# Kernel optimization log

Measured on AMD Instinct MI355X. Metric: run time of the kernel, lower is better.

## Reference

```python
import jax, jax.numpy as jnp
import numpy as np

N_NODES = 100000
N_EDGES = 1600000
D_FEAT = 128
D_EMB = 128
ROUNDS = 4
M_OUT = 32
NUM_GRAPHS = 512


def setup_inputs() -> dict:
    key = jax.random.key(0)
    ks = jax.random.split(key, 12)
    x = jax.random.normal(ks[0], (N_NODES, D_FEAT), dtype=jnp.float32)
    edge_index = jax.random.randint(ks[1], (2, N_EDGES), 0, N_NODES, dtype=jnp.int32)
    batch = jnp.sort(jax.random.randint(ks[2], (N_NODES,), 0, NUM_GRAPHS, dtype=jnp.int32))
    s = 1.0 / np.sqrt(D_EMB)
    emb_W = jax.random.uniform(ks[3], (D_FEAT, D_EMB), minval=-s, maxval=s, dtype=jnp.float32)
    emb_b = jax.random.uniform(ks[4], (D_EMB,), minval=-s, maxval=s, dtype=jnp.float32)
    msg_W = jax.random.uniform(ks[5], (ROUNDS, D_EMB, D_EMB), minval=-s, maxval=s, dtype=jnp.float32)
    msg_b = jax.random.uniform(ks[6], (ROUNDS, D_EMB), minval=-s, maxval=s, dtype=jnp.float32)
    upd_W = jax.random.uniform(ks[7], (ROUNDS, D_EMB, D_EMB), minval=-s, maxval=s, dtype=jnp.float32)
    upd_b = jax.random.uniform(ks[8], (ROUNDS, D_EMB), minval=-s, maxval=s, dtype=jnp.float32)
    out_W = jax.random.uniform(ks[9], (D_EMB, M_OUT), minval=-s, maxval=s, dtype=jnp.float32)
    out_b = jax.random.uniform(ks[10], (M_OUT,), minval=-s, maxval=s, dtype=jnp.float32)
    return {"x": x, "edge_index": edge_index, "batch": batch,
            "emb_W": emb_W, "emb_b": emb_b, "msg_W": msg_W, "msg_b": msg_b,
            "upd_W": upd_W, "upd_b": upd_b, "out_W": out_W, "out_b": out_b}


def reference(x, edge_index, batch, emb_W, emb_b, msg_W, msg_b, upd_W, upd_b, out_W, out_b):
    src, dst = edge_index[0], edge_index[1]
    # initial node embedding: Linear + ReLU
    state = jax.nn.relu(x @ emb_W + emb_b)  # [N, D]
    for r in range(ROUNDS):
        message = jax.nn.relu(state @ msg_W[r] + msg_b[r])      # [N, D]
        # gather messages along edges, scatter-add to destination nodes
        aggregated = jax.ops.segment_sum(message[src], dst, num_segments=N_NODES)  # [N, D]
        state = state + jax.nn.relu(aggregated @ upd_W[r] + upd_b[r])
    # sum-pool nodes into graphs
    graph_state = jax.ops.segment_sum(state, batch, num_segments=NUM_GRAPHS)  # [G, D]
    return graph_state @ out_W + out_b  # [G, M]
```

## Files before the change

kernel.cpp:

```cpp
#include <hip/hip_runtime.h>

#define N_NODES    100000
#define N_EDGES    1600000
#define D_EMB      128
#define ROUNDS     4
#define M_OUT      32
#define NUM_GRAPHS 512

#define N_TILES    (N_NODES / 32)
#define GEMM_BLOCKS 1024

#define NPASS      8
#define PASS_RANGE (N_NODES / NPASS)

#define SCAN_ELEMS_PER_BLOCK 1024
#define SCAN_NBLK ((N_NODES + SCAN_ELEMS_PER_BLOCK - 1) / SCAN_ELEMS_PER_BLOCK)

typedef __attribute__((ext_vector_type(8))) short short8;
typedef __attribute__((ext_vector_type(4))) float f32x4;

static __device__ __forceinline__ unsigned short f2bf(float f) {
    union { float f; unsigned u; } v; v.f = f;
    unsigned u = v.u;
    unsigned r = (u + 0x7FFFu + ((u >> 16) & 1u)) >> 16;
    return (unsigned short)r;
}
static __device__ __forceinline__ float bf2f(unsigned short h) {
    union { unsigned u; float f; } v; v.u = ((unsigned)h) << 16;
    return v.f;
}

__global__ __launch_bounds__(256) void prep_weights_kernel(
    const float* __restrict__ emb_W, const float* __restrict__ msg_W,
    const float* __restrict__ upd_W, unsigned short* __restrict__ WTall)
{
    const int mi = blockIdx.x;
    const float* W = (mi == 0) ? emb_W
                   : (mi <= 4) ? msg_W + (size_t)(mi - 1) * D_EMB * D_EMB
                               : upd_W + (size_t)(mi - 5) * D_EMB * D_EMB;
    unsigned short* WT = WTall + (size_t)mi * D_EMB * D_EMB;
    for (int idx = threadIdx.x; idx < D_EMB * D_EMB; idx += 256) {
        const int n = idx >> 7, k = idx & 127;
        WT[idx] = f2bf(W[k * D_EMB + n]);
    }
}

template<int MODE, bool AF32>
__global__ __launch_bounds__(256) void gemm_loop_kernel(
    const void* __restrict__ Aptr, const unsigned short* __restrict__ WT,
    const float* __restrict__ bias, unsigned short* __restrict__ state,
    unsigned short* __restrict__ outb)
{
    __shared__ unsigned short As[2][32][136];

    const int tid  = threadIdx.x;
    const int lane = tid & 63;
    const int w    = tid >> 6;
    const int m    = lane & 15;
    const int g    = lane >> 4;

    short8 bfr[2][4];
    #pragma unroll
    for (int ct = 0; ct < 2; ++ct) {
        const int n = w * 32 + ct * 16 + m;
        #pragma unroll
        for (int ks = 0; ks < 4; ++ks)
            bfr[ct][ks] = *(const short8*)&WT[n * D_EMB + ks * 32 + g * 8];
    }
    const float bv0 = bias[w * 32 + m];
    const float bv1 = bias[w * 32 + 16 + m];

    int tile = blockIdx.x;

    if (AF32) {
        const float4* A4 = (const float4*)Aptr;
        #pragma unroll
        for (int i = 0; i < 4; ++i) {
            const int ch = tid + (i << 8);
            const float4 f = A4[(size_t)tile * 1024 + ch];
            ushort4 h; h.x = f2bf(f.x); h.y = f2bf(f.y); h.z = f2bf(f.z); h.w = f2bf(f.w);
            *(ushort4*)&As[0][ch >> 5][(ch & 31) << 2] = h;
        }
    } else {
        const uint4* A2 = (const uint4*)Aptr;
        #pragma unroll
        for (int i = 0; i < 2; ++i) {
            const int ch = tid + (i << 8);
            const uint4 v = A2[(size_t)tile * 512 + ch];
            *(uint4*)&As[0][ch >> 4][(ch & 15) << 3] = v;
        }
    }
    __syncthreads();

    int cur = 0;
    while (true) {
        const int next = tile + GEMM_BLOCKS;
        const bool have = next < N_TILES;

        float4 rgf[4]; uint4 rgu[2];
        if (have) {
            if (AF32) {
                const float4* A4 = (const float4*)Aptr;
                #pragma unroll
                for (int i = 0; i < 4; ++i)
                    rgf[i] = A4[(size_t)next * 1024 + tid + (i << 8)];
            } else {
                const uint4* A2 = (const uint4*)Aptr;
                #pragma unroll
                for (int i = 0; i < 2; ++i)
                    rgu[i] = A2[(size_t)next * 512 + tid + (i << 8)];
            }
        }

        short8 a[2][4];
        #pragma unroll
        for (int rt = 0; rt < 2; ++rt)
            #pragma unroll
            for (int ks = 0; ks < 4; ++ks)
                a[rt][ks] = *(const short8*)&As[cur][rt * 16 + m][ks * 32 + g * 8];

        f32x4 acc[2][2] = {};
        #pragma unroll
        for (int ks = 0; ks < 4; ++ks)
            #pragma unroll
            for (int rt = 0; rt < 2; ++rt)
                #pragma unroll
                for (int ct = 0; ct < 2; ++ct)
                    acc[rt][ct] = __builtin_amdgcn_mfma_f32_16x16x32_bf16(
                        a[rt][ks], bfr[ct][ks], acc[rt][ct], 0, 0, 0);

        if (have) {
            if (AF32) {
                #pragma unroll
                for (int i = 0; i < 4; ++i) {
                    const int ch = tid + (i << 8);
                    ushort4 h;
                    h.x = f2bf(rgf[i].x); h.y = f2bf(rgf[i].y);
                    h.z = f2bf(rgf[i].z); h.w = f2bf(rgf[i].w);
                    *(ushort4*)&As[cur ^ 1][ch >> 5][(ch & 31) << 2] = h;
                }
            } else {
                #pragma unroll
                for (int i = 0; i < 2; ++i) {
                    const int ch = tid + (i << 8);
                    *(uint4*)&As[cur ^ 1][ch >> 4][(ch & 15) << 3] = rgu[i];
                }
            }
        }

        #pragma unroll
        for (int rt = 0; rt < 2; ++rt) {
            #pragma unroll
            for (int ct = 0; ct < 2; ++ct) {
                const int col = w * 32 + ct * 16 + m;
                const float bv = ct ? bv1 : bv0;
                #pragma unroll
                for (int r = 0; r < 4; ++r) {
                    const int row = tile * 32 + rt * 16 + g * 4 + r;
                    const size_t idx = (size_t)row * D_EMB + col;
                    const float v = fmaxf(acc[rt][ct][r] + bv, 0.f);
                    if (MODE == 0) outb[idx] = f2bf(v);
                    else           state[idx] = f2bf(v);
                }
            }
        }

        if (!have) break;
        __syncthreads();
        cur ^= 1;
        tile = next;
    }
}

__global__ __launch_bounds__(256) void hist_mp_kernel(
    const int* __restrict__ dst, int* __restrict__ deg)
{
    const int p = blockIdx.x & 7;
    const int e = (blockIdx.x >> 3) * 256 + threadIdx.x;
    const int d = dst[e];
    if ((unsigned)(d - p * PASS_RANGE) < (unsigned)PASS_RANGE)
        atomicAdd(&deg[d], 1);
}

__global__ __launch_bounds__(256) void scan_local_kernel(
    const int* __restrict__ deg, int* __restrict__ rp, int* __restrict__ partials)
{
    __shared__ int sm[256];
    const int tid  = threadIdx.x;
    const int base = blockIdx.x * SCAN_ELEMS_PER_BLOCK + tid * 4;

    int v0 = (base + 0 < N_NODES) ? deg[base + 0] : 0;
    int v1 = (base + 1 < N_NODES) ? deg[base + 1] : 0;
    int v2 = (base + 2 < N_NODES) ? deg[base + 2] : 0;
    int v3 = (base + 3 < N_NODES) ? deg[base + 3] : 0;
    const int tot = v0 + v1 + v2 + v3;

    sm[tid] = tot;
    __syncthreads();
    #pragma unroll
    for (int off = 1; off < 256; off <<= 1) {
        const int x = (tid >= off) ? sm[tid - off] : 0;
        __syncthreads();
        sm[tid] += x;
        __syncthreads();
    }
    const int bex = sm[tid] - tot;

    if (base + 0 < N_NODES) rp[base + 0] = bex;
    if (base + 1 < N_NODES) rp[base + 1] = bex + v0;
    if (base + 2 < N_NODES) rp[base + 2] = bex + v0 + v1;
    if (base + 3 < N_NODES) rp[base + 3] = bex + v0 + v1 + v2;
    if (tid == 255) partials[blockIdx.x] = sm[255];
}

__global__ __launch_bounds__(128) void scan_partials_kernel(int* __restrict__ partials)
{
    __shared__ int sm[128];
    const int tid = threadIdx.x;
    const int v = (tid < SCAN_NBLK) ? partials[tid] : 0;
    sm[tid] = v;
    __syncthreads();
    #pragma unroll
    for (int off = 1; off < 128; off <<= 1) {
        const int x = (tid >= off) ? sm[tid - off] : 0;
        __syncthreads();
        sm[tid] += x;
        __syncthreads();
    }
    if (tid < SCAN_NBLK) partials[tid] = sm[tid] - v;
}

__global__ __launch_bounds__(256) void scan_fixup_kernel(
    int* __restrict__ rp, const int* __restrict__ partials, int* __restrict__ pos)
{
    const int i = blockIdx.x * 256 + threadIdx.x;
    if (i < N_NODES) {
        const int v = rp[i] + partials[i >> 10];
        rp[i] = v;
        pos[i] = v;
    }
    if (i == 0) rp[N_NODES] = N_EDGES;
}

__global__ __launch_bounds__(256) void fill_mp_kernel(
    const int* __restrict__ src, const int* __restrict__ dst,
    int* __restrict__ pos, int* __restrict__ esrc)
{
    const int p = blockIdx.x & 7;
    const int e = (blockIdx.x >> 3) * 256 + threadIdx.x;
    const int d = dst[e];
    if ((unsigned)(d - p * PASS_RANGE) < (unsigned)PASS_RANGE) {
        const int idx = atomicAdd(&pos[d], 1);
        esrc[idx] = src[e];
    }
}

__global__ __launch_bounds__(256) void fused_upd_kernel(
    const unsigned short* __restrict__ msg, const int* __restrict__ rp,
    const int* __restrict__ esrc, const unsigned short* __restrict__ WT,
    const float* __restrict__ bias, unsigned short* __restrict__ state)
{
    __shared__ unsigned short As[32][136];
    __shared__ int wq;

    const int tid  = threadIdx.x;
    const int lane = tid & 63;
    const int wid  = tid >> 6;
    const int m    = lane & 15;
    const int g    = lane >> 4;
    const int b    = blockIdx.x;
    const int j    = tid & 15;

    if (tid == 0) wq = 0;

    short8 bfr[2][4];
    #pragma unroll
    for (int ct = 0; ct < 2; ++ct) {
        const int n = wid * 32 + ct * 16 + m;
        #pragma unroll
        for (int ks = 0; ks < 4; ++ks)
            bfr[ct][ks] = *(const short8*)&WT[n * D_EMB + ks * 32 + g * 8];
    }
    const float bv0 = bias[wid * 32 + m];
    const float bv1 = bias[wid * 32 + 16 + m];

    __syncthreads();

    const uint4* m4 = (const uint4*)msg;

    while (true) {
        int t = 0;
        if (j == 0) t = atomicAdd(&wq, 1);
        t = __shfl(t, lane & 48, 64);
        if (t >= 32) break;

        const int n = b * 32 + t;
        const int beg = rp[n];
        const int end = rp[n + 1];

        float a0[8] = {0,0,0,0,0,0,0,0};
        float a1[8] = {0,0,0,0,0,0,0,0};
        int i = beg;
        for (; i + 3 < end; i += 4) {
            const uint4 v0 = m4[(size_t)esrc[i]     * 16 + j];
            const uint4 v1 = m4[(size_t)esrc[i + 1] * 16 + j];
            const uint4 v2 = m4[(size_t)esrc[i + 2] * 16 + j];
            const uint4 v3 = m4[(size_t)esrc[i + 3] * 16 + j];
            a0[0] += bf2f(v0.x & 0xffff); a0[1] += bf2f(v0.x >> 16);
            a0[2] += bf2f(v0.y & 0xffff); a0[3] += bf2f(v0.y >> 16);
            a0[4] += bf2f(v0.z & 0xffff); a0[5] += bf2f(v0.z >> 16);
            a0[6] += bf2f(v0.w & 0xffff); a0[7] += bf2f(v0.w >> 16);
            a1[0] += bf2f(v1.x & 0xffff); a1[1] += bf2f(v1.x >> 16);
            a1[2] += bf2f(v1.y & 0xffff); a1[3] += bf2f(v1.y >> 16);
            a1[4] += bf2f(v1.z & 0xffff); a1[5] += bf2f(v1.z >> 16);
            a1[6] += bf2f(v1.w & 0xffff); a1[7] += bf2f(v1.w >> 16);
            a0[0] += bf2f(v2.x & 0xffff); a0[1] += bf2f(v2.x >> 16);
            a0[2] += bf2f(v2.y & 0xffff); a0[3] += bf2f(v2.y >> 16);
            a0[4] += bf2f(v2.z & 0xffff); a0[5] += bf2f(v2.z >> 16);
            a0[6] += bf2f(v2.w & 0xffff); a0[7] += bf2f(v2.w >> 16);
            a1[0] += bf2f(v3.x & 0xffff); a1[1] += bf2f(v3.x >> 16);
            a1[2] += bf2f(v3.y & 0xffff); a1[3] += bf2f(v3.y >> 16);
            a1[4] += bf2f(v3.z & 0xffff); a1[5] += bf2f(v3.z >> 16);
            a1[6] += bf2f(v3.w & 0xffff); a1[7] += bf2f(v3.w >> 16);
        }
        for (; i < end; ++i) {
            const uint4 v0 = m4[(size_t)esrc[i] * 16 + j];
            a0[0] += bf2f(v0.x & 0xffff); a0[1] += bf2f(v0.x >> 16);
            a0[2] += bf2f(v0.y & 0xffff); a0[3] += bf2f(v0.y >> 16);
            a0[4] += bf2f(v0.z & 0xffff); a0[5] += bf2f(v0.z >> 16);
            a0[6] += bf2f(v0.w & 0xffff); a0[7] += bf2f(v0.w >> 16);
        }
        #pragma unroll
        for (int q = 0; q < 8; ++q) a0[q] += a1[q];

        uint4 o;
        o.x = (unsigned)f2bf(a0[0]) | ((unsigned)f2bf(a0[1]) << 16);
        o.y = (unsigned)f2bf(a0[2]) | ((unsigned)f2bf(a0[3]) << 16);
        o.z = (unsigned)f2bf(a0[4]) | ((unsigned)f2bf(a0[5]) << 16);
        o.w = (unsigned)f2bf(a0[6]) | ((unsigned)f2bf(a0[7]) << 16);
        *(uint4*)&As[t][j * 8] = o;
    }
    __syncthreads();

    short8 a[2][4];
    #pragma unroll
    for (int rt = 0; rt < 2; ++rt)
        #pragma unroll
        for (int ks = 0; ks < 4; ++ks)
            a[rt][ks] = *(const short8*)&As[rt * 16 + m][ks * 32 + g * 8];

    f32x4 acc[2][2] = {};
    #pragma unroll
    for (int ks = 0; ks < 4; ++ks)
        #pragma unroll
        for (int rt = 0; rt < 2; ++rt)
            #pragma unroll
            for (int ct = 0; ct < 2; ++ct)
                acc[rt][ct] = __builtin_amdgcn_mfma_f32_16x16x32_bf16(
                    a[rt][ks], bfr[ct][ks], acc[rt][ct], 0, 0, 0);

    #pragma unroll
    for (int rt = 0; rt < 2; ++rt) {
        #pragma unroll
        for (int ct = 0; ct < 2; ++ct) {
            const int col = wid * 32 + ct * 16 + m;
            const float bv = ct ? bv1 : bv0;
            #pragma unroll
            for (int r = 0; r < 4; ++r) {
                const int row = b * 32 + rt * 16 + g * 4 + r;
                const size_t idx = (size_t)row * D_EMB + col;
                const float v = fmaxf(acc[rt][ct][r] + bv, 0.f);
                state[idx] = f2bf(bf2f(state[idx]) + v);
            }
        }
    }
}

__global__ __launch_bounds__(256) void pool_kernel(
    const unsigned short* __restrict__ state, const int* __restrict__ batch,
    float* __restrict__ gs)
{
    const int lane = threadIdx.x & 63;
    const int grp  = threadIdx.x >> 6;
    const int n0 = blockIdx.x * 128 + grp * 32;
    const int c0 = lane * 2;

    float a0 = 0.f, a1 = 0.f;
    int cur = -1;
    for (int i = 0; i < 32; ++i) {
        const int n = n0 + i;
        if (n >= N_NODES) break;
        const int bb = batch[n];
        if (bb != cur) {
            if (cur >= 0) {
                unsafeAtomicAdd(&gs[cur * D_EMB + c0],     a0);
                unsafeAtomicAdd(&gs[cur * D_EMB + c0 + 1], a1);
            }
            cur = bb; a0 = 0.f; a1 = 0.f;
        }
        const unsigned u = *(const unsigned*)&state[(size_t)n * D_EMB + c0];
        a0 += bf2f(u & 0xffff);
        a1 += bf2f(u >> 16);
    }
    if (cur >= 0) {
        unsafeAtomicAdd(&gs[cur * D_EMB + c0],     a0);
        unsafeAtomicAdd(&gs[cur * D_EMB + c0 + 1], a1);
    }
}

__global__ __launch_bounds__(256) void out_kernel(
    const float* __restrict__ gs, const float* __restrict__ W,
    const float* __restrict__ bias, float* __restrict__ out)
{
    const int idx = blockIdx.x * 256 + threadIdx.x;
    const int g = idx >> 5;
    const int m = idx & 31;
    float acc = 0.f;
    #pragma unroll 8
    for (int k = 0; k < D_EMB; ++k)
        acc += gs[g * D_EMB + k] * W[k * M_OUT + m];
    out[idx] = acc + bias[m];
}

extern "C" void kernel_launch(void* const* d_in, const int* in_sizes, int n_in,
                              void* d_out, int out_size, void* d_ws, size_t ws_size,
                              hipStream_t stream)
{
    const float* x     = (const float*)d_in[0];
    const int*   eidx  = (const int*)d_in[1];
    const int*   batch = (const int*)d_in[2];
    const float* emb_W = (const float*)d_in[3];
    const float* emb_b = (const float*)d_in[4];
    const float* msg_W = (const float*)d_in[5];
    const float* msg_b = (const float*)d_in[6];
    const float* upd_W = (const float*)d_in[7];
    const float* upd_b = (const float*)d_in[8];
    const float* out_W = (const float*)d_in[9];
    const float* out_b = (const float*)d_in[10];
    float* out = (float*)d_out;

    const int* src = eidx;
    const int* dst = eidx + N_EDGES;

    char* p = (char*)d_ws;
    unsigned short* state = (unsigned short*)p;   p += (size_t)N_NODES * D_EMB * 2;
    unsigned short* msg   = (unsigned short*)p;   p += (size_t)N_NODES * D_EMB * 2;
    float* gs = (float*)p;                        p += (size_t)NUM_GRAPHS * D_EMB * 4;
    unsigned short* WTall = (unsigned short*)p;   p += (size_t)9 * D_EMB * D_EMB * 2;
    int* rp   = (int*)p;                          p += (size_t)(N_NODES + 1) * 4;
    int* deg  = (int*)p;                          p += (size_t)N_NODES * 4;
    int* pos  = (int*)p;                          p += (size_t)N_NODES * 4;
    int* partials = (int*)p;                      p += (size_t)128 * 4;
    int* esrc = (int*)p;                          p += (size_t)N_EDGES * 4;

    const dim3 blk(256);
    const int mp_grid = (N_EDGES / 256) * NPASS;

    prep_weights_kernel<<<9, blk, 0, stream>>>(emb_W, msg_W, upd_W, WTall);
    hipMemsetAsync(deg, 0, (size_t)N_NODES * sizeof(int), stream);
    hist_mp_kernel<<<mp_grid, blk, 0, stream>>>(dst, deg);
    scan_local_kernel<<<SCAN_NBLK, blk, 0, stream>>>(deg, rp, partials);
    scan_partials_kernel<<<1, 128, 0, stream>>>(partials);
    scan_fixup_kernel<<<(SCAN_NBLK * SCAN_ELEMS_PER_BLOCK) / 256, blk, 0, stream>>>(rp, partials, pos);
    fill_mp_kernel<<<mp_grid, blk, 0, stream>>>(src, dst, pos, esrc);

    gemm_loop_kernel<2, true><<<GEMM_BLOCKS, blk, 0, stream>>>(
        x, WTall, emb_b, state, nullptr);

    for (int r = 0; r < ROUNDS; ++r) {
        gemm_loop_kernel<0, false><<<GEMM_BLOCKS, blk, 0, stream>>>(
            state, WTall + (size_t)(1 + r) * D_EMB * D_EMB,
            msg_b + (size_t)r * D_EMB, nullptr, msg);
        fused_upd_kernel<<<N_TILES, blk, 0, stream>>>(
            msg, rp, esrc, WTall + (size_t)(5 + r) * D_EMB * D_EMB,
            upd_b + (size_t)r * D_EMB, state);
    }

    hipMemsetAsync(gs, 0, (size_t)NUM_GRAPHS * D_EMB * sizeof(float), stream);
    pool_kernel<<<(N_NODES + 127) / 128, blk, 0, stream>>>(state, batch, gs);
    out_kernel<<<(NUM_GRAPHS * M_OUT) / 256, blk, 0, stream>>>(gs, out_W, out_b, out);
}
```

Before: 599.9 us.

## Unroll gather to 8 edges, add nontemporal index loads, raise GEMM grid

```diff
diff --git a/kernel.cpp b/kernel.cpp
--- a/kernel.cpp
+++ b/kernel.cpp
@@ -8,7 +8,7 @@
 #define NUM_GRAPHS 512
 
 #define N_TILES    (N_NODES / 32)
-#define GEMM_BLOCKS 1024
+#define GEMM_BLOCKS 1568
 
 #define NPASS      8
 #define PASS_RANGE (N_NODES / NPASS)
@@ -71,6 +71,7 @@
     const float bv1 = bias[w * 32 + 16 + m];
 
     int tile = blockIdx.x;
+    if (tile >= N_TILES) return;
 
     if (AF32) {
         const float4* A4 = (const float4*)Aptr;
@@ -177,7 +178,7 @@
 {
     const int p = blockIdx.x & 7;
     const int e = (blockIdx.x >> 3) * 256 + threadIdx.x;
-    const int d = dst[e];
+    const int d = __builtin_nontemporal_load(&dst[e]);
     if ((unsigned)(d - p * PASS_RANGE) < (unsigned)PASS_RANGE)
         atomicAdd(&deg[d], 1);
 }
@@ -248,10 +249,11 @@
 {
     const int p = blockIdx.x & 7;
     const int e = (blockIdx.x >> 3) * 256 + threadIdx.x;
-    const int d = dst[e];
+    const int d = __builtin_nontemporal_load(&dst[e]);
     if ((unsigned)(d - p * PASS_RANGE) < (unsigned)PASS_RANGE) {
+        const int s = __builtin_nontemporal_load(&src[e]);
         const int idx = atomicAdd(&pos[d], 1);
-        esrc[idx] = src[e];
+        esrc[idx] = s;
     }
 }
 
@@ -301,27 +303,40 @@
         float a0[8] = {0,0,0,0,0,0,0,0};
         float a1[8] = {0,0,0,0,0,0,0,0};
         int i = beg;
-        for (; i + 3 < end; i += 4) {
-            const uint4 v0 = m4[(size_t)esrc[i]     * 16 + j];
-            const uint4 v1 = m4[(size_t)esrc[i + 1] * 16 + j];
-            const uint4 v2 = m4[(size_t)esrc[i + 2] * 16 + j];
-            const uint4 v3 = m4[(size_t)esrc[i + 3] * 16 + j];
-            a0[0] += bf2f(v0.x & 0xffff); a0[1] += bf2f(v0.x >> 16);
-            a0[2] += bf2f(v0.y & 0xffff); a0[3] += bf2f(v0.y >> 16);
-            a0[4] += bf2f(v0.z & 0xffff); a0[5] += bf2f(v0.z >> 16);
-            a0[6] += bf2f(v0.w & 0xffff); a0[7] += bf2f(v0.w >> 16);
-            a1[0] += bf2f(v1.x & 0xffff); a1[1] += bf2f(v1.x >> 16);
-            a1[2] += bf2f(v1.y & 0xffff); a1[3] += bf2f(v1.y >> 16);
-            a1[4] += bf2f(v1.z & 0xffff); a1[5] += bf2f(v1.z >> 16);
-            a1[6] += bf2f(v1.w & 0xffff); a1[7] += bf2f(v1.w >> 16);
-            a0[0] += bf2f(v2.x & 0xffff); a0[1] += bf2f(v2.x >> 16);
-            a0[2] += bf2f(v2.y & 0xffff); a0[3] += bf2f(v2.y >> 16);
-            a0[4] += bf2f(v2.z & 0xffff); a0[5] += bf2f(v2.z >> 16);
-            a0[6] += bf2f(v2.w & 0xffff); a0[7] += bf2f(v2.w >> 16);
-            a1[0] += bf2f(v3.x & 0xffff); a1[1] += bf2f(v3.x >> 16);
-            a1[2] += bf2f(v3.y & 0xffff); a1[3] += bf2f(v3.y >> 16);
-            a1[4] += bf2f(v3.z & 0xffff); a1[5] += bf2f(v3.z >> 16);
-            a1[6] += bf2f(v3.w & 0xffff); a1[7] += bf2f(v3.w >> 16);
+        for (; i + 7 < end; i += 8) {
+            uint4 v[8];
+            #pragma unroll
+            for (int q = 0; q < 8; ++q)
+                v[q] = m4[(size_t)esrc[i + q] * 16 + j];
+            #pragma unroll
+            for (int q = 0; q < 8; q += 2) {
+                a0[0] += bf2f(v[q].x & 0xffff); a0[1] += bf2f(v[q].x >> 16);
+                a0[2] += bf2f(v[q].y & 0xffff); a0[3] += bf2f(v[q].y >> 16);
+                a0[4] += bf2f(v[q].z & 0xffff); a0[5] += bf2f(v[q].z >> 16);
+                a0[6] += bf2f(v[q].w & 0xffff); a0[7] += bf2f(v[q].w >> 16);
+                a1[0] += bf2f(v[q+1].x & 0xffff); a1[1] += bf2f(v[q+1].x >> 16);
+                a1[2] += bf2f(v[q+1].y & 0xffff); a1[3] += bf2f(v[q+1].y >> 16);
+                a1[4] += bf2f(v[q+1].z & 0xffff); a1[5] += bf2f(v[q+1].z >> 16);
+                a1[6] += bf2f(v[q+1].w & 0xffff); a1[7] += bf2f(v[q+1].w >> 16);
+            }
+        }
+        if (i + 3 < end) {
+            uint4 v[4];
+            #pragma unroll
+            for (int q = 0; q < 4; ++q)
+                v[q] = m4[(size_t)esrc[i + q] * 16 + j];
+            #pragma unroll
+            for (int q = 0; q < 4; q += 2) {
+                a0[0] += bf2f(v[q].x & 0xffff); a0[1] += bf2f(v[q].x >> 16);
+                a0[2] += bf2f(v[q].y & 0xffff); a0[3] += bf2f(v[q].y >> 16);
+                a0[4] += bf2f(v[q].z & 0xffff); a0[5] += bf2f(v[q].z >> 16);
+                a0[6] += bf2f(v[q].w & 0xffff); a0[7] += bf2f(v[q].w >> 16);
+                a1[0] += bf2f(v[q+1].x & 0xffff); a1[1] += bf2f(v[q+1].x >> 16);
+                a1[2] += bf2f(v[q+1].y & 0xffff); a1[3] += bf2f(v[q+1].y >> 16);
+                a1[4] += bf2f(v[q+1].z & 0xffff); a1[5] += bf2f(v[q+1].z >> 16);
+                a1[6] += bf2f(v[q+1].w & 0xffff); a1[7] += bf2f(v[q+1].w >> 16);
+            }
+            i += 4;
         }
         for (; i < end; ++i) {
             const uint4 v0 = m4[(size_t)esrc[i] * 16 + j];
```

Result: no change. 603.3 us (+0.6%).
